# Optimization experiments

Hardware: AMD Instinct MI355X
Metric: run time of the kernel (lower is better)

## Reference

```python
import jax, jax.numpy as jnp
import numpy as np

# regular 3x3 kernel grid: row0 = dy (i-1), row1 = dx (j-1), k = 3*i + j
RY = jnp.array([-1., -1., -1., 0., 0., 0., 1., 1., 1.], dtype=jnp.float32)
RX = jnp.array([-1., 0., 1., -1., 0., 1., -1., 0., 1.], dtype=jnp.float32)


def conv2d(x, w, b):
    # 3x3, stride 1, pad 1, NCHW/OIHW
    out = jax.lax.conv_general_dilated(
        x, w, window_strides=(1, 1), padding=((1, 1), (1, 1)),
        dimension_numbers=('NCHW', 'OIHW', 'NCHW'))
    return out + b[None, :, None, None]


def group_norm(x, gamma, beta, num_groups, eps=1e-5):
    N, C, H, W = x.shape
    xg = x.reshape(N, num_groups, C // num_groups, H, W)
    mu = xg.mean(axis=(2, 3, 4), keepdims=True)
    var = xg.var(axis=(2, 3, 4), keepdims=True)
    xn = ((xg - mu) * jax.lax.rsqrt(var + eps)).reshape(N, C, H, W)
    return xn * gamma[None, :, None, None] + beta[None, :, None, None]


def build_offset(tm, tr):
    # tm: [N,4,H,W] per-pixel 2x2 affine [[m00,m01],[m10,m11]]; tr: [N,2,H,W] (ty, tx)
    m00, m01, m10, m11 = tm[:, 0], tm[:, 1], tm[:, 2], tm[:, 3]  # [N,H,W]
    ry = RY[None, :, None, None]
    rx = RX[None, :, None, None]
    # offset = M @ R - R, plus translation broadcast to all 9 points
    dy = m00[:, None] * ry + m01[:, None] * rx - ry + tr[:, 0:1]  # [N,9,H,W]
    dx = m10[:, None] * ry + m11[:, None] * rx - rx + tr[:, 1:2]  # [N,9,H,W]
    return dy, dx


def bilinear_sample(img, py, px):
    # img: [N,C,H,W]; py, px: [N,K,H,W] sampling locations; zero padding outside
    N, C, H, W = img.shape
    K = py.shape[1]
    y0f = jnp.floor(py)
    x0f = jnp.floor(px)
    wy1 = py - y0f
    wx1 = px - x0f
    wy0 = 1.0 - wy1
    wx0 = 1.0 - wx1
    y0 = y0f.astype(jnp.int32)
    x0 = x0f.astype(jnp.int32)
    img_flat = img.reshape(N, C, H * W)

    def gather(yi, xi):
        valid = ((yi >= 0) & (yi < H) & (xi >= 0) & (xi < W)).astype(img.dtype)
        idx = jnp.clip(yi, 0, H - 1) * W + jnp.clip(xi, 0, W - 1)  # [N,K,H,W]
        flat = idx.reshape(N, 1, K * H * W)
        vals = jnp.take_along_axis(img_flat, jnp.broadcast_to(flat, (N, C, K * H * W)), axis=2)
        return vals.reshape(N, C, K, H, W) * valid[:, None]

    v00 = gather(y0, x0)
    v01 = gather(y0, x0 + 1)
    v10 = gather(y0 + 1, x0)
    v11 = gather(y0 + 1, x0 + 1)
    return (v00 * (wy0 * wx0)[:, None] + v01 * (wy0 * wx1)[:, None]
            + v10 * (wy1 * wx0)[:, None] + v11 * (wy1 * wx1)[:, None])


def deform_conv(x, dy, dx, w, pad=1, dil=1):
    # x: [N,Cin,H,W]; dy,dx: [N,9,H,W]; w: [Cout,Cin,3,3]; stride 1
    N, C, H, W = x.shape
    k = jnp.arange(9)
    ki = (k // 3).astype(x.dtype)[None, :, None, None]
    kj = (k % 3).astype(x.dtype)[None, :, None, None]
    hh = jnp.arange(H, dtype=x.dtype)[None, None, :, None]
    ww = jnp.arange(W, dtype=x.dtype)[None, None, None, :]
    py = hh - pad + dil * ki + dy  # [N,9,H,W]
    px = ww - pad + dil * kj + dx
    sampled = bilinear_sample(x, py, px)  # [N,C,9,H,W]
    return jnp.einsum('nckhw,ock->nohw', sampled, w.reshape(w.shape[0], C, 9))


def setup_inputs() -> dict:
    key = jax.random.key(0)
    ks = jax.random.split(key, 16)
    N, C, H, W = 4, 256, 64, 64
    x = jax.random.normal(ks[0], (N, C, H, W), jnp.float32)
    def p(k, shape, s):
        return jax.random.normal(k, shape, jnp.float32) * s
    s_off = 0.01                       # small STN heads -> modest offsets
    s_dc = 1.0 / np.sqrt(C * 9.0)      # deform-conv fan-in init
    return {
        'x': x,
        'w_tm1': p(ks[1], (4, C, 3, 3), s_off), 'b_tm1': jnp.zeros((4,), jnp.float32),
        'w_tr1': p(ks[2], (2, C, 3, 3), s_off), 'b_tr1': jnp.zeros((2,), jnp.float32),
        'w_dc1': p(ks[3], (C, C, 3, 3), s_dc),
        'g1': jnp.ones((C,), jnp.float32), 'be1': jnp.zeros((C,), jnp.float32),
        'w_tm2': p(ks[4], (4, C, 3, 3), s_off), 'b_tm2': jnp.zeros((4,), jnp.float32),
        'w_tr2': p(ks[5], (2, C, 3, 3), s_off), 'b_tr2': jnp.zeros((2,), jnp.float32),
        'w_dc2': p(ks[6], (C, C, 3, 3), s_dc),
        'g2': jnp.ones((C,), jnp.float32), 'be2': jnp.zeros((C,), jnp.float32),
    }


def reference(x, w_tm1, b_tm1, w_tr1, b_tr1, w_dc1, g1, be1,
              w_tm2, b_tm2, w_tr2, b_tr2, w_dc2, g2, be2):
    GROUPS = 32
    residual = x
    dy1, dx1 = build_offset(conv2d(x, w_tm1, b_tm1), conv2d(x, w_tr1, b_tr1))
    out = deform_conv(x, dy1, dx1, w_dc1)
    out = jax.nn.relu(group_norm(out, g1, be1, GROUPS))
    dy2, dx2 = build_offset(conv2d(out, w_tm2, b_tm2), conv2d(out, w_tr2, b_tr2))
    out = deform_conv(out, dy2, dx2, w_dc2)
    out = group_norm(out, g2, be2, GROUPS)
    return jax.nn.relu(out + residual)
```

## Files before the change

kernel.cpp:

```cpp
#include <hip/hip_runtime.h>


typedef unsigned int u32;
typedef unsigned short u16;
typedef __attribute__((ext_vector_type(8))) short bf16x8;
typedef __attribute__((ext_vector_type(4))) float floatx4;

#define HW 4096
#define CHW 1048576

static __device__ __forceinline__ float bf2f(u16 u) {
    union { u32 i; float f; } c; c.i = ((u32)u) << 16; return c.f;
}
static __device__ __forceinline__ u16 f2bf(float f) {
    union { float f; u32 i; } c; c.f = f;
    u32 x = c.i;
    return (u16)((x + 0x7FFFu + ((x >> 16) & 1u)) >> 16);
}
static __device__ __forceinline__ u32 cvtpk(float a, float b) {
    u32 r;
    asm("v_cvt_pk_bf16_f32 %0, %1, %2" : "=v"(r) : "v"(a), "v"(b));
    return r;
}
static __device__ __forceinline__ float loadv(const void* p, long i, int f32) {
    return f32 ? ((const float*)p)[i] : bf2f(((const u16*)p)[i]);
}
static __device__ __forceinline__ int sniff_f32(const u32* __restrict__ xw) {
    int cnt = 0;
    #pragma unroll
    for (int s = 0; s < 16; ++s) {
        union { u32 i; float f; } c;
        c.i = xw[s * 131 + 7];
        float a = fabsf(c.f);
        if (a > 1e-8f && a < 1e4f) ++cnt;
    }
    return (cnt >= 8) ? 1 : 0;
}

__global__ __launch_bounds__(256) void k_prep_all(
    const void* __restrict__ x,
    const void* __restrict__ wdc1, const void* __restrict__ wdc2,
    const void* __restrict__ wtm1, const void* __restrict__ wtr1,
    const void* __restrict__ wtm2, const void* __restrict__ wtr2,
    u16* __restrict__ xT, u16* __restrict__ wTg1, u16* __restrict__ wTg2,
    u16* __restrict__ wT61, u16* __restrict__ wT62)
{
    __shared__ u16 T[64 * 258];
    const int f32 = sniff_f32((const u32*)x);
    const int b = blockIdx.x;
    const int tid = threadIdx.x;

    if (b < 256) {
        const int n = b >> 6, h = b & 63;
        const long sb = (long)n * CHW + (h << 6);
        const int cb = tid >> 3;
        const int w0 = (tid & 7) << 3;
        if (f32) {
            const float* xp = (const float*)x;
            for (int it = 0; it < 8; ++it) {
                int c = (it << 5) + cb;
                const float* pr = xp + sb + (long)c * HW + w0;
                float4 a = ((const float4*)pr)[0];
                float4 d = ((const float4*)pr)[1];
                T[(w0 + 0) * 258 + c] = f2bf(a.x);
                T[(w0 + 1) * 258 + c] = f2bf(a.y);
                T[(w0 + 2) * 258 + c] = f2bf(a.z);
                T[(w0 + 3) * 258 + c] = f2bf(a.w);
                T[(w0 + 4) * 258 + c] = f2bf(d.x);
                T[(w0 + 5) * 258 + c] = f2bf(d.y);
                T[(w0 + 6) * 258 + c] = f2bf(d.z);
                T[(w0 + 7) * 258 + c] = f2bf(d.w);
            }
        } else {
            const u16* xp = (const u16*)x;
            for (int it = 0; it < 8; ++it) {
                int c = (it << 5) + cb;
                uint4 v = *(const uint4*)(xp + sb + (long)c * HW + w0);
                u32 ws[4] = {v.x, v.y, v.z, v.w};
                #pragma unroll
                for (int q = 0; q < 4; ++q) {
                    T[(w0 + 2 * q + 0) * 258 + c] = (u16)(ws[q] & 0xFFFFu);
                    T[(w0 + 2 * q + 1) * 258 + c] = (u16)(ws[q] >> 16);
                }
            }
        }
        __syncthreads();
        const int w = tid >> 2, cq = tid & 3;
        const u32* Tr = (const u32*)T;
        u16* ob = xT + (long)n * CHW + (long)((h << 6) + w) * 256 + cq * 64;
        #pragma unroll
        for (int s = 0; s < 8; ++s) {
            uint4 o;
            o.x = Tr[129 * w + 32 * cq + 4 * s + 0];
            o.y = Tr[129 * w + 32 * cq + 4 * s + 1];
            o.z = Tr[129 * w + 32 * cq + 4 * s + 2];
            o.w = Tr[129 * w + 32 * cq + 4 * s + 3];
            *(uint4*)&ob[s * 8] = o;
        }
    } else if (b < 2560) {
        const int r2 = (b >= 1408);
        const void* wdc = r2 ? wdc2 : wdc1;
        u16* wTg = r2 ? wTg2 : wTg1;
        int idx2 = (b - (r2 ? 1408 : 256)) * 256 + tid;
        int cp = idx2 & 15;
        int o  = (idx2 >> 4) & 255;
        int q  = idx2 >> 12;
        int k  = q >> 3;
        int c0 = ((q & 7) << 5) + (cp << 1);
        long s0 = (long)o * 2304 + c0 * 9 + k;
        ((u32*)wTg)[idx2] = cvtpk(loadv(wdc, s0, f32), loadv(wdc, s0 + 9, f32));
    } else {
        const int r2 = (b >= 2704);
        const void* wtm = r2 ? wtm2 : wtm1;
        const void* wtr = r2 ? wtr2 : wtr1;
        u16* wT6 = r2 ? wT62 : wT61;
        int i = (b - (r2 ? 2704 : 2560)) * 256 + tid;
        int q  = i >> 9;
        int o  = (i >> 5) & 15;
        int cc = i & 31;
        int k  = q >> 3;
        int c  = ((q & 7) << 5) + cc;
        float v = 0.f;
        if (o < 4)      v = loadv(wtm, (long)o * 2304 + c * 9 + k, f32);
        else if (o < 6) v = loadv(wtr, (long)(o - 4) * 2304 + c * 9 + k, f32);
        wT6[i] = f2bf(v);
    }
}

__global__ __launch_bounds__(512, 4) void k_deform(
    const u16* __restrict__ srcT, const u16* __restrict__ wTg,
    const u16* __restrict__ wT6,
    const void* __restrict__ b_tm, const void* __restrict__ b_tr,
    const u32* __restrict__ xw,
    u16* __restrict__ raw, float* __restrict__ pstats)
{
    __shared__ float red[8][32][17];
    __shared__ float tl[6 * 32];
    __shared__ __align__(16) short Sl[2][32 * 40];
    __shared__ int   g_y0[288];
    __shared__ int   g_x0[288];
    __shared__ float g_wy[288];
    __shared__ float g_wx[288];

    const int tid = threadIdx.x;
    const int bid = blockIdx.x;
    const int n = bid >> 7, h = (bid >> 1) & 63, half = bid & 1;
    const int wb = half << 5;
    const int lane = tid & 63;
    const int quad = lane >> 4;
    const int l16  = lane & 15;
    const int wv   = tid >> 6;
    const long nbase = (long)n * CHW;
    const u16* sp = srcT + nbase;

    {
        floatx4 acc6[2];
        acc6[0] = (floatx4){0.f, 0.f, 0.f, 0.f};
        acc6[1] = (floatx4){0.f, 0.f, 0.f, 0.f};
        for (int qi = 0; qi < 9; ++qi) {
            const int q = wv * 9 + qi;
            const int k = q >> 3, cb = q & 7;
            const int ky = k / 3, kx = k % 3;
            const int row = h + ky - 1;
            const bool rv = (row >= 0) && (row < 64);
            bf16x8 av = *(const bf16x8*)&wT6[(((q << 4) + l16) << 5) + (quad << 3)];
            #pragma unroll
            for (int j = 0; j < 2; ++j) {
                int psrc = wb + (j << 4) + l16 + kx - 1;
                bf16x8 bv = {0, 0, 0, 0, 0, 0, 0, 0};
                if (rv && psrc >= 0 && psrc < 64)
                    bv = *(const bf16x8*)&sp[(((long)(row << 6) + psrc) << 8) + (cb << 5) + (quad << 3)];
                acc6[j] = __builtin_amdgcn_mfma_f32_16x16x32_bf16(av, bv, acc6[j], 0, 0, 0);
            }
        }
        #pragma unroll
        for (int j = 0; j < 2; ++j)
            #pragma unroll
            for (int r = 0; r < 4; ++r)
                red[wv][(j << 4) + l16][(quad << 2) + r] = acc6[j][r];
        __syncthreads();
        if (tid < 192) {
            const int o = tid >> 5, px = tid & 31;
            float s = 0.f;
            #pragma unroll
            for (int v = 0; v < 8; ++v) s += red[v][px][o];
            const int f32 = sniff_f32(xw);
            float bias = (o < 4) ? loadv(b_tm, o, f32) : loadv(b_tr, o - 4, f32);
            tl[o * 32 + px] = s + bias;
        }
        __syncthreads();
    }

    for (int i = tid; i < 288; i += 512) {
        int k = i >> 5, ww2 = i & 31;
        float m00 = tl[ww2],       m01 = tl[32 + ww2];
        float m10 = tl[64 + ww2],  m11 = tl[96 + ww2];
        float tr0 = tl[128 + ww2], tr1 = tl[160 + ww2];
        float ry = (float)(k / 3) - 1.f;
        float rx = (float)(k % 3) - 1.f;
        float dy = m00 * ry + m01 * rx - ry + tr0;
        float dx = m10 * ry + m11 * rx - rx + tr1;
        float py = (float)h + ry + dy;
        float px = (float)(wb + ww2) + rx + dx;
        float y0f = floorf(py), x0f = floorf(px);
        g_y0[i] = (int)y0f; g_x0[i] = (int)x0f;
        g_wy[i] = py - y0f; g_wx[i] = px - x0f;
    }
    __syncthreads();

    const int sw  = tid >> 4;
    const int scq = tid & 15;
    const int o0  = wv << 5;

    floatx4 acc[2][2];
    #pragma unroll
    for (int i = 0; i < 2; ++i)
        #pragma unroll
        for (int j = 0; j < 2; ++j)
            acc[i][j] = (floatx4){0.f, 0.f, 0.f, 0.f};

    int ld_k = -1;
    int a00 = 0, a01 = 0, a10 = 0, a11 = 0;
    int pb_k = -1;
    float cw00 = 0.f, cw01 = 0.f, cw10 = 0.f, cw11 = 0.f;

    auto ld_addr = [&](int k) {
        int gi = (k << 5) + sw;
        int y0 = g_y0[gi], x0 = g_x0[gi];
        int yc0 = min(max(y0, 0), 63),     yc1 = min(max(y0 + 1, 0), 63);
        int xc0 = min(max(x0, 0), 63),     xc1 = min(max(x0 + 1, 0), 63);
        a00 = yc0 * 64 + xc0; a01 = yc0 * 64 + xc1;
        a10 = yc1 * 64 + xc0; a11 = yc1 * 64 + xc1;
    };
    auto pb_w = [&](int k) {
        int gi = (k << 5) + sw;
        int y0 = g_y0[gi], x0 = g_x0[gi];
        float wy1 = g_wy[gi], wx1 = g_wx[gi];
        float wy0 = 1.f - wy1, wx0 = 1.f - wx1;
        bool yv0 = (y0 >= 0) && (y0 < 64);
        bool yv1 = (y0 >= -1) && (y0 < 63);
        bool xv0 = (x0 >= 0) && (x0 < 64);
        bool xv1 = (x0 >= -1) && (x0 < 63);
        cw00 = (yv0 && xv0) ? wy0 * wx0 : 0.f;
        cw01 = (yv0 && xv1) ? wy0 * wx1 : 0.f;
        cw10 = (yv1 && xv0) ? wy1 * wx0 : 0.f;
        cw11 = (yv1 && xv1) ? wy1 * wx1 : 0.f;
    };
    auto smp = [&](int q, u32& r00, u32& r01, u32& r10, u32& r11) {
        int k = q >> 3;
        if (k != ld_k) { ld_k = k; ld_addr(k); }
        const int cc = ((q & 7) << 5) + (scq << 1);
        r00 = *(const u32*)&sp[(long)a00 * 256 + cc];
        r01 = *(const u32*)&sp[(long)a01 * 256 + cc];
        r10 = *(const u32*)&sp[(long)a10 * 256 + cc];
        r11 = *(const u32*)&sp[(long)a11 * 256 + cc];
    };
    auto wload = [&](int q, bf16x8& W0, bf16x8& W1) {
        const u16* wp = wTg + (((size_t)q * 256 + o0 + l16) << 5) + (quad << 3);
        W0 = *(const bf16x8*)wp;
        W1 = *(const bf16x8*)(wp + (16 << 5));
    };
    auto pub = [&](int q, int b, u32 r00, u32 r01, u32 r10, u32 r11) {
        int k = q >> 3;
        if (k != pb_k) { pb_k = k; pb_w(k); }
        float va = fmaf(cw00, bf2f((u16)r00),
                   fmaf(cw01, bf2f((u16)r01),
                   fmaf(cw10, bf2f((u16)r10), cw11 * bf2f((u16)r11))));
        float vb = fmaf(cw00, bf2f((u16)(r00 >> 16)),
                   fmaf(cw01, bf2f((u16)(r01 >> 16)),
                   fmaf(cw10, bf2f((u16)(r10 >> 16)), cw11 * bf2f((u16)(r11 >> 16)))));
        *(u32*)&Sl[b][sw * 40 + (scq << 1)] = cvtpk(va, vb);
    };
    auto mfma4 = [&](int b, bf16x8 W0, bf16x8 W1) {
        #pragma unroll
        for (int j = 0; j < 2; ++j) {
            bf16x8 bv = *(const bf16x8*)&Sl[b][((j << 4) + l16) * 40 + (quad << 3)];
            acc[0][j] = __builtin_amdgcn_mfma_f32_16x16x32_bf16(W0, bv, acc[0][j], 0, 0, 0);
            acc[1][j] = __builtin_amdgcn_mfma_f32_16x16x32_bf16(W1, bv, acc[1][j], 0, 0, 0);
        }
    };

    u32 sA0, sA1, sA2, sA3, sB0, sB1, sB2, sB3;
    bf16x8 WA0, WA1, WB0, WB1;

    smp(0, sA0, sA1, sA2, sA3);
    smp(1, sB0, sB1, sB2, sB3);
    wload(0, WA0, WA1);
    wload(1, WB0, WB1);
    pub(0, 0, sA0, sA1, sA2, sA3);
    __syncthreads();

    for (int q = 0; q < 72; q += 2) {
        if (q + 2 < 72) smp(q + 2, sA0, sA1, sA2, sA3);
        mfma4(0, WA0, WA1);
        pub(q + 1, 1, sB0, sB1, sB2, sB3);
        if (q + 2 < 72) wload(q + 2, WA0, WA1);
        __syncthreads();

        if (q + 3 < 72) smp(q + 3, sB0, sB1, sB2, sB3);
        mfma4(1, WB0, WB1);
        if (q + 2 < 72) pub(q + 2, 0, sA0, sA1, sA2, sA3);
        if (q + 3 < 72) wload(q + 3, WB0, WB1);
        __syncthreads();
    }

    #pragma unroll
    for (int i = 0; i < 2; ++i) {
        float s1 = 0.f, s2 = 0.f;
        #pragma unroll
        for (int j = 0; j < 2; ++j)
            #pragma unroll
            for (int r = 0; r < 4; ++r) {
                float v = acc[i][j][r];
                s1 += v; s2 += v * v;
            }
        #pragma unroll
        for (int off = 1; off <= 16; off <<= 1) {
            s1 += __shfl_xor(s1, off, 64);
            s2 += __shfl_xor(s2, off, 64);
        }
        if ((lane & 31) == 0) {
            int g = (o0 >> 3) + 2 * i + (lane >> 5);
            pstats[((long)bid << 6) + (g << 1)]     = s1;
            pstats[((long)bid << 6) + (g << 1) + 1] = s2;
        }
    }

    #pragma unroll
    for (int i = 0; i < 2; ++i)
        #pragma unroll
        for (int j = 0; j < 2; ++j)
            #pragma unroll
            for (int r = 0; r < 4; ++r) {
                int o = o0 + i * 16 + quad * 4 + r;
                raw[nbase + ((long)o << 12) + (h << 6) + wb + (j << 4) + l16]
                    = f2bf(acc[i][j][r]);
            }
}

__global__ __launch_bounds__(256) void k_gn_relu(
    const u16* __restrict__ raw, const float* __restrict__ pstats,
    const void* __restrict__ gamma, const void* __restrict__ beta,
    const u32* __restrict__ xw,
    u16* __restrict__ out1)
{
    __shared__ u16 T[64 * 258];
    __shared__ float sred[4][64];
    __shared__ float sl[64];
    const int f32 = sniff_f32(xw);
    const int bid = blockIdx.x;
    const int n = bid >> 6, h = bid & 63;
    const int tid = threadIdx.x;

    {
        const int v = tid & 63, part = tid >> 6;
        float a = 0.f;
        for (int j = part * 32; j < part * 32 + 32; ++j)
            a += pstats[(((long)n * 128 + j) << 6) + v];
        sred[part][v] = a;
        __syncthreads();
        if (tid < 64) sl[tid] = sred[0][tid] + sred[1][tid] + sred[2][tid] + sred[3][tid];
        __syncthreads();
    }

    const u16* rb = raw + (long)n * CHW + (h << 6);
    const int cb = tid >> 3;
    const int w0 = (tid & 7) << 3;
    for (int it = 0; it < 8; ++it) {
        int c = (it << 5) + cb;
        int g = c >> 3;
        float mean = sl[g * 2] * (1.f / 32768.f);
        float var  = sl[g * 2 + 1] * (1.f / 32768.f) - mean * mean;
        float rstd = rsqrtf(var + 1e-5f);
        float ga = loadv(gamma, c, f32) * rstd;
        float be = loadv(beta, c, f32) - mean * ga;
        uint4 v = *(const uint4*)(rb + (long)c * HW + w0);
        u32 ws[4] = {v.x, v.y, v.z, v.w};
        #pragma unroll
        for (int q = 0; q < 4; ++q) {
            float a = fmaxf(fmaf(bf2f((u16)(ws[q] & 0xFFFFu)), ga, be), 0.f);
            float b = fmaxf(fmaf(bf2f((u16)(ws[q] >> 16)),     ga, be), 0.f);
            T[(w0 + 2 * q + 0) * 258 + c] = f2bf(a);
            T[(w0 + 2 * q + 1) * 258 + c] = f2bf(b);
        }
    }
    __syncthreads();
    const int w = tid >> 2, cq = tid & 3;
    const u32* Tr = (const u32*)T;
    u16* ob = out1 + (long)n * CHW + (long)((h << 6) + w) * 256 + cq * 64;
    #pragma unroll
    for (int s = 0; s < 8; ++s) {
        uint4 o;
        o.x = Tr[129 * w + 32 * cq + 4 * s + 0];
        o.y = Tr[129 * w + 32 * cq + 4 * s + 1];
        o.z = Tr[129 * w + 32 * cq + 4 * s + 2];
        o.w = Tr[129 * w + 32 * cq + 4 * s + 3];
        *(uint4*)&ob[s * 8] = o;
    }
}

__global__ __launch_bounds__(256) void k_gn_final(
    const u16* __restrict__ raw, const float* __restrict__ pstats,
    const void* __restrict__ gamma, const void* __restrict__ beta,
    const void* __restrict__ x,
    void* __restrict__ outp)
{
    __shared__ float rr[256];
    const int f32 = sniff_f32((const u32*)x);
    const int tid = threadIdx.x;
    const long e0 = ((long)blockIdx.x) << 11;
    const int n = (int)(e0 >> 20);
    const int c0 = (int)((e0 >> 12) & 255);
    const int g = c0 >> 3;

    {
        int j = tid & 127, sv = tid >> 7;
        rr[tid] = pstats[(((long)n * 128 + j) << 6) + (g << 1) + sv];
        __syncthreads();
        #pragma unroll
        for (int s = 64; s >= 1; s >>= 1) {
            if ((tid & 127) < s) rr[tid] += rr[tid + s];
            __syncthreads();
        }
    }
    float mean = rr[0] * (1.f / 32768.f);
    float var  = rr[128] * (1.f / 32768.f) - mean * mean;
    float rstd = rsqrtf(var + 1e-5f);

    const long i = blockIdx.x * 256 + tid;
    const long e = i << 3;
    const int c = (int)((e >> 12) & 255);
    float ga = loadv(gamma, c, f32) * rstd;
    float be = loadv(beta, c, f32) - mean * ga;
    uint4 p = ((const uint4*)raw)[i];
    u32 ww[4] = {p.x, p.y, p.z, p.w};
    float v[8];
    #pragma unroll
    for (int q = 0; q < 4; ++q) {
        v[2 * q + 0] = fmaxf(fmaf(bf2f((u16)(ww[q] & 0xFFFFu)), ga, be) + loadv(x, e + 2 * q + 0, f32), 0.f);
        v[2 * q + 1] = fmaxf(fmaf(bf2f((u16)(ww[q] >> 16)),     ga, be) + loadv(x, e + 2 * q + 1, f32), 0.f);
    }
    if (f32) {
        float4* op = (float4*)((float*)outp + e);
        op[0] = make_float4(v[0], v[1], v[2], v[3]);
        op[1] = make_float4(v[4], v[5], v[6], v[7]);
    } else {
        uint4 o;
        o.x = cvtpk(v[0], v[1]);
        o.y = cvtpk(v[2], v[3]);
        o.z = cvtpk(v[4], v[5]);
        o.w = cvtpk(v[6], v[7]);
        ((uint4*)outp)[i] = o;
    }
}

extern "C" void kernel_launch(void* const* d_in, const int* in_sizes, int n_in,
                              void* d_out, int out_size, void* d_ws, size_t ws_size,
                              hipStream_t stream) {
    const void* x     = d_in[0];
    const void* w_tm1 = d_in[1];
    const void* b_tm1 = d_in[2];
    const void* w_tr1 = d_in[3];
    const void* b_tr1 = d_in[4];
    const void* w_dc1 = d_in[5];
    const void* g1    = d_in[6];
    const void* be1   = d_in[7];
    const void* w_tm2 = d_in[8];
    const void* b_tm2 = d_in[9];
    const void* w_tr2 = d_in[10];
    const void* b_tr2 = d_in[11];
    const void* w_dc2 = d_in[12];
    const void* g2    = d_in[13];
    const void* be2   = d_in[14];

    char* wsb = (char*)d_ws;
    u16*   xT     = (u16*)wsb;
    u16*   raw    = (u16*)(wsb + 8388608);
    u16*   wTg1   = (u16*)(wsb + 16777216);
    u16*   wTg2   = (u16*)(wsb + 17956864);
    u16*   wT61   = (u16*)(wsb + 19136512);
    u16*   wT62   = (u16*)(wsb + 19210240);
    float* pstats = (float*)(wsb + 19283968);
    u16*   out1   = xT;
    const u32* xw = (const u32*)x;

    k_prep_all<<<2848, 256, 0, stream>>>(x, w_dc1, w_dc2, w_tm1, w_tr1, w_tm2, w_tr2,
                                         xT, wTg1, wTg2, wT61, wT62);
    k_deform  <<<512, 512, 0, stream>>>(xT, wTg1, wT61, b_tm1, b_tr1, xw, raw, pstats);
    k_gn_relu <<<256, 256, 0, stream>>>(raw, pstats, g1, be1, xw, out1);
    k_deform  <<<512, 512, 0, stream>>>(out1, wTg2, wT62, b_tm2, b_tr2, xw, raw, pstats);
    k_gn_final<<<2048, 256, 0, stream>>>(raw, pstats, g2, be2, x, d_out);
}
```

Before: 249.6 us.

## Deepen software pipeline of deformable conv sampling with unrolled per-tap loop

Restructures the main deformable-conv loop into an outer loop over the 9 taps and a fully unrolled inner loop over 8 channel blocks. Sample loads are issued three steps ahead and weight loads two steps ahead, using register ring buffers, while LDS reads are hoisted before the MFMAs. Per-tap address and bilinear-weight computation move to fixed points in the unrolled loop, replacing the per-iteration tap checks, and precomputed pointers replace index arithmetic. The aim is to hide global-load latency better and cut scalar overhead, at the cost of more live registers and possibly lower occupancy.

```diff
diff --git a/kernel.cpp b/kernel.cpp
--- a/kernel.cpp
+++ b/kernel.cpp
@@ -219,20 +219,26 @@
         for (int j = 0; j < 2; ++j)
             acc[i][j] = (floatx4){0.f, 0.f, 0.f, 0.f};
 
-    int ld_k = -1;
-    int a00 = 0, a01 = 0, a10 = 0, a11 = 0;
-    int pb_k = -1;
-    float cw00 = 0.f, cw01 = 0.f, cw10 = 0.f, cw11 = 0.f;
-
-    auto ld_addr = [&](int k) {
+    short* slw = &Sl[0][sw * 40 + (scq << 1)];
+    const short* slr = &Sl[0][l16 * 40 + (quad << 3)];
+    const int wlane = ((o0 + l16) << 5) + (quad << 3);
+    const u16* wq = wTg;
+
+    const u16* p00; const u16* p01; const u16* p10; const u16* p11;
+    float cw00, cw01, cw10, cw11;
+
+    auto mkptr = [&](int k) {
         int gi = (k << 5) + sw;
         int y0 = g_y0[gi], x0 = g_x0[gi];
         int yc0 = min(max(y0, 0), 63),     yc1 = min(max(y0 + 1, 0), 63);
         int xc0 = min(max(x0, 0), 63),     xc1 = min(max(x0 + 1, 0), 63);
-        a00 = yc0 * 64 + xc0; a01 = yc0 * 64 + xc1;
-        a10 = yc1 * 64 + xc0; a11 = yc1 * 64 + xc1;
+        const u16* bp = sp + (scq << 1);
+        p00 = bp + (((yc0 << 6) + xc0) << 8);
+        p01 = bp + (((yc0 << 6) + xc1) << 8);
+        p10 = bp + (((yc1 << 6) + xc0) << 8);
+        p11 = bp + (((yc1 << 6) + xc1) << 8);
     };
-    auto pb_w = [&](int k) {
+    auto mkcw = [&](int k) {
         int gi = (k << 5) + sw;
         int y0 = g_y0[gi], x0 = g_x0[gi];
         float wy1 = g_wy[gi], wx1 = g_wx[gi];
@@ -246,62 +252,69 @@
         cw10 = (yv1 && xv0) ? wy1 * wx0 : 0.f;
         cw11 = (yv1 && xv1) ? wy1 * wx1 : 0.f;
     };
-    auto smp = [&](int q, u32& r00, u32& r01, u32& r10, u32& r11) {
-        int k = q >> 3;
-        if (k != ld_k) { ld_k = k; ld_addr(k); }
-        const int cc = ((q & 7) << 5) + (scq << 1);
-        r00 = *(const u32*)&sp[(long)a00 * 256 + cc];
-        r01 = *(const u32*)&sp[(long)a01 * 256 + cc];
-        r10 = *(const u32*)&sp[(long)a10 * 256 + cc];
-        r11 = *(const u32*)&sp[(long)a11 * 256 + cc];
+
+    u32 S[4][4];
+    bf16x8 W0[4], W1[4];
+
+    auto SMP = [&](int cb, int set) {
+        S[set][0] = *(const u32*)(p00 + (cb << 5));
+        S[set][1] = *(const u32*)(p01 + (cb << 5));
+        S[set][2] = *(const u32*)(p10 + (cb << 5));
+        S[set][3] = *(const u32*)(p11 + (cb << 5));
     };
-    auto wload = [&](int q, bf16x8& W0, bf16x8& W1) {
-        const u16* wp = wTg + (((size_t)q * 256 + o0 + l16) << 5) + (quad << 3);
-        W0 = *(const bf16x8*)wp;
-        W1 = *(const bf16x8*)(wp + (16 << 5));
+    auto WLD = [&](int slot) {
+        W0[slot] = *(const bf16x8*)(wq + wlane);
+        W1[slot] = *(const bf16x8*)(wq + wlane + 512);
+        wq += 8192;
     };
-    auto pub = [&](int q, int b, u32 r00, u32 r01, u32 r10, u32 r11) {
-        int k = q >> 3;
-        if (k != pb_k) { pb_k = k; pb_w(k); }
+    auto PUB = [&](int set, int slot) {
+        u32 r00 = S[set][0], r01 = S[set][1], r10 = S[set][2], r11 = S[set][3];
         float va = fmaf(cw00, bf2f((u16)r00),
                    fmaf(cw01, bf2f((u16)r01),
                    fmaf(cw10, bf2f((u16)r10), cw11 * bf2f((u16)r11))));
         float vb = fmaf(cw00, bf2f((u16)(r00 >> 16)),
                    fmaf(cw01, bf2f((u16)(r01 >> 16)),
                    fmaf(cw10, bf2f((u16)(r10 >> 16)), cw11 * bf2f((u16)(r11 >> 16)))));
-        *(u32*)&Sl[b][sw * 40 + (scq << 1)] = cvtpk(va, vb);
+        *(u32*)(slw + slot * 1280) = cvtpk(va, vb);
     };
-    auto mfma4 = [&](int b, bf16x8 W0, bf16x8 W1) {
-        #pragma unroll
-        for (int j = 0; j < 2; ++j) {
-            bf16x8 bv = *(const bf16x8*)&Sl[b][((j << 4) + l16) * 40 + (quad << 3)];
-            acc[0][j] = __builtin_amdgcn_mfma_f32_16x16x32_bf16(W0, bv, acc[0][j], 0, 0, 0);
-            acc[1][j] = __builtin_amdgcn_mfma_f32_16x16x32_bf16(W1, bv, acc[1][j], 0, 0, 0);
-        }
+    auto MFMA4 = [&](int ws, bf16x8 b0, bf16x8 b1) {
+        acc[0][0] = __builtin_amdgcn_mfma_f32_16x16x32_bf16(W0[ws], b0, acc[0][0], 0, 0, 0);
+        acc[1][0] = __builtin_amdgcn_mfma_f32_16x16x32_bf16(W1[ws], b0, acc[1][0], 0, 0, 0);
+        acc[0][1] = __builtin_amdgcn_mfma_f32_16x16x32_bf16(W0[ws], b1, acc[0][1], 0, 0, 0);
+        acc[1][1] = __builtin_amdgcn_mfma_f32_16x16x32_bf16(W1[ws], b1, acc[1][1], 0, 0, 0);
     };
 
-    u32 sA0, sA1, sA2, sA3, sB0, sB1, sB2, sB3;
-    bf16x8 WA0, WA1, WB0, WB1;
-
-    smp(0, sA0, sA1, sA2, sA3);
-    smp(1, sB0, sB1, sB2, sB3);
-    wload(0, WA0, WA1);
-    wload(1, WB0, WB1);
-    pub(0, 0, sA0, sA1, sA2, sA3);
+    mkptr(0); mkcw(0);
+    SMP(0, 0); SMP(1, 1); SMP(2, 2);
+    WLD(0); WLD(1);
+    PUB(0, 0);
     __syncthreads();
 
-    for (int q = 0; q < 72; q += 2) {
-        if (q + 2 < 72) smp(q + 2, sA0, sA1, sA2, sA3);
-        mfma4(0, WA0, WA1);
-        pub(q + 1, 1, sB0, sB1, sB2, sB3);
-        if (q + 2 < 72) wload(q + 2, WA0, WA1);
-        __syncthreads();
-
-        if (q + 3 < 72) smp(q + 3, sB0, sB1, sB2, sB3);
-        mfma4(1, WB0, WB1);
-        if (q + 2 < 72) pub(q + 2, 0, sA0, sA1, sA2, sA3);
-        if (q + 3 < 72) wload(q + 3, WB0, WB1);
-        __syncthreads();
+    for (int k8 = 0; k8 < 8; ++k8) {
+        #pragma unroll
+        for (int c = 0; c < 8; ++c) {
+            const int sl = c & 1;
+            bf16x8 b0 = *(const bf16x8*)(slr + sl * 1280);
+            bf16x8 b1 = *(const bf16x8*)(slr + sl * 1280 + 640);
+            if (c == 5) mkptr(k8 + 1);
+            SMP((c + 3) & 7, (c + 3) & 3);
+            WLD((c + 2) & 3);
+            if (c == 7) mkcw(k8 + 1);
+            PUB((c + 1) & 3, (c + 1) & 1);
+            MFMA4(c & 3, b0, b1);
+            __syncthreads();
+        }
+    }
+    #pragma unroll
+    for (int c = 0; c < 8; ++c) {
+        const int sl = c & 1;
+        bf16x8 b0 = *(const bf16x8*)(slr + sl * 1280);
+        bf16x8 b1 = *(const bf16x8*)(slr + sl * 1280 + 640);
+        if (c < 5) SMP((c + 3) & 7, (c + 3) & 3);
+        if (c < 6) WLD((c + 2) & 3);
+        if (c < 7) PUB((c + 1) & 3, (c + 1) & 1);
+        MFMA4(c & 3, b0, b1);
+        if (c < 7) __syncthreads();
     }
 
     #pragma unroll
```

Result: faster. 236.8 us (-5.1%).
